# Kernel optimization log

Hardware: AMD Instinct MI355X
Metric: run time of the kernel (lower is better)

The kernel has to match this reference:

```python
import jax, jax.numpy as jnp
import numpy as np

NUM_HEADS = 8

def setup_inputs() -> dict:
    key = jax.random.key(0)
    k1, k2, k3, k4 = jax.random.split(key, 4)
    B, N, C = 2, 4096, 768
    x = jax.random.normal(k1, (B, N, C), dtype=jnp.float32)
    w_qkv = jax.random.normal(k2, (C, 3 * C), dtype=jnp.float32) * (C ** -0.5)
    w_proj = jax.random.normal(k3, (C, C), dtype=jnp.float32) * (C ** -0.5)
    b_proj = jax.random.normal(k4, (C,), dtype=jnp.float32) * 0.02
    return {"x": x, "w_qkv": w_qkv, "w_proj": w_proj, "b_proj": b_proj}

def reference(x, w_qkv, w_proj, b_proj):
    B, N, C = x.shape
    H = NUM_HEADS
    Dh = C // H
    scale = Dh ** -0.5
    # qkv: [B, N, 3C] -> [B, N, 3, H, Dh] -> [3, B, H, N, Dh]
    qkv = (x @ w_qkv).reshape(B, N, 3, H, Dh).transpose(2, 0, 3, 1, 4)
    q, k, v = qkv[0], qkv[1], qkv[2]
    attn = jnp.einsum('bhqd,bhkd->bhqk', q, k) * scale  # [B,H,N,N]
    attn = jax.nn.softmax(attn, axis=-1)
    out = jnp.einsum('bhqk,bhkd->bhqd', attn, v)        # [B,H,N,Dh]
    out = out.transpose(0, 2, 1, 3).reshape(B, N, C)
    return out @ w_proj + b_proj
```

## Files before the change

### kernel.cpp

```cpp
#include <hip/hip_runtime.h>
#include <hip/hip_bf16.h>

typedef __attribute__((ext_vector_type(8))) short short8;
typedef __attribute__((ext_vector_type(4))) short short4v;
typedef __attribute__((ext_vector_type(4))) float f32x4;
typedef __attribute__((ext_vector_type(16))) float f32x16;

#define MFMA16(a,b,c) __builtin_amdgcn_mfma_f32_16x16x32_bf16(a,b,c,0,0,0)
#define MFMA32(a,b,c) __builtin_amdgcn_mfma_f32_32x32x16_bf16(a,b,c,0,0,0)

__device__ __forceinline__ unsigned short f2b_rne(float f){
  union { float f; unsigned int u; } v; v.f = f;
  unsigned int u = v.u;
  return (unsigned short)((u + 0x7FFFu + ((u >> 16) & 1u)) >> 16);
}

__device__ __forceinline__ short8 pack8f(float4 a, float4 b){
  short8 o;
  o[0] = (short)f2b_rne(a.x); o[1] = (short)f2b_rne(a.y);
  o[2] = (short)f2b_rne(a.z); o[3] = (short)f2b_rne(a.w);
  o[4] = (short)f2b_rne(b.x); o[5] = (short)f2b_rne(b.y);
  o[6] = (short)f2b_rne(b.z); o[7] = (short)f2b_rne(b.w);
  return o;
}

__device__ __forceinline__ f32x16 zero16(){
  f32x16 z;
  #pragma unroll
  for (int i = 0; i < 16; ++i) z[i] = 0.f;
  return z;
}

__global__ void k_transpose_cvt2(const float* __restrict__ wqkv, const float* __restrict__ wproj,
                                 unsigned short* __restrict__ oqkv, unsigned short* __restrict__ oproj){
  __shared__ unsigned short tile[32][33];
  const float* in; unsigned short* out; int Cc;
  if (blockIdx.z == 0){ in = wqkv; out = oqkv; Cc = 2304; }
  else {
    if (blockIdx.x >= 24) return;
    in = wproj; out = oproj; Cc = 768;
  }
  int c0 = blockIdx.x * 32, r0 = blockIdx.y * 32;
  int tx = threadIdx.x, ty = threadIdx.y;
  #pragma unroll
  for (int i = 0; i < 32; i += 8)
    tile[ty + i][tx] = f2b_rne(in[(size_t)(r0 + ty + i) * Cc + c0 + tx]);
  __syncthreads();
  #pragma unroll
  for (int i = 0; i < 32; i += 8)
    out[(size_t)(c0 + ty + i) * 768 + r0 + tx] = tile[tx][ty + i];
}

__global__ __launch_bounds__(256) void k_gemm_qkv(
    const float* __restrict__ X,
    const unsigned short* __restrict__ Bt,
    unsigned short* __restrict__ qbuf,
    unsigned short* __restrict__ kbuf,
    unsigned short* __restrict__ vtb)
{
  __shared__ short As[128 * 40];
  __shared__ short Bs[128 * 40];
  int m0 = blockIdx.x * 128, n0 = blockIdx.y * 128;
  int t = threadIdx.x, l = t & 63, w = t >> 6;
  int lr = l & 15, lh = l >> 4;
  int wr = w >> 1, wc = w & 1;

  int row0 = t >> 2, cs0 = t & 3;
  int row1 = row0 + 64;
  const float* ga0 = X + (size_t)(m0 + row0) * 768 + cs0 * 8;
  const float* ga1 = X + (size_t)(m0 + row1) * 768 + cs0 * 8;
  const unsigned short* gb0 = Bt + (size_t)(n0 + row0) * 768 + cs0 * 8;
  const unsigned short* gb1 = Bt + (size_t)(n0 + row1) * 768 + cs0 * 8;
  short* la0 = As + row0 * 40 + cs0 * 8;
  short* la1 = As + row1 * 40 + cs0 * 8;
  short* lb0 = Bs + row0 * 40 + cs0 * 8;
  short* lb1 = Bs + row1 * 40 + cs0 * 8;

  f32x4 acc[4][4];
  f32x4 z4 = {0.f, 0.f, 0.f, 0.f};
  #pragma unroll
  for (int mf = 0; mf < 4; ++mf)
    #pragma unroll
    for (int nf = 0; nf < 4; ++nf) acc[mf][nf] = z4;

  float4 fa0 = *(const float4*)ga0, fa0b = *(const float4*)(ga0 + 4);
  float4 fa1 = *(const float4*)ga1, fa1b = *(const float4*)(ga1 + 4);
  short8 rb0 = *(const short8*)gb0;
  short8 rb1 = *(const short8*)gb1;

  for (int kt = 0; kt < 24; ++kt){
    short8 ra0 = pack8f(fa0, fa0b);
    short8 ra1 = pack8f(fa1, fa1b);
    __syncthreads();
    *(short8*)la0 = ra0; *(short8*)la1 = ra1;
    *(short8*)lb0 = rb0; *(short8*)lb1 = rb1;
    __syncthreads();
    if (kt < 23){
      fa0 = *(const float4*)(ga0 + (kt + 1) * 32); fa0b = *(const float4*)(ga0 + (kt + 1) * 32 + 4);
      fa1 = *(const float4*)(ga1 + (kt + 1) * 32); fa1b = *(const float4*)(ga1 + (kt + 1) * 32 + 4);
      rb0 = *(const short8*)(gb0 + (kt + 1) * 32);
      rb1 = *(const short8*)(gb1 + (kt + 1) * 32);
    }
    short8 af[4], bfm[4];
    #pragma unroll
    for (int mf = 0; mf < 4; ++mf)
      af[mf] = *(const short8*)(As + (wr * 64 + mf * 16 + lr) * 40 + lh * 8);
    #pragma unroll
    for (int nf = 0; nf < 4; ++nf)
      bfm[nf] = *(const short8*)(Bs + (wc * 64 + nf * 16 + lr) * 40 + lh * 8);
    #pragma unroll
    for (int mf = 0; mf < 4; ++mf)
      #pragma unroll
      for (int nf = 0; nf < 4; ++nf)
        acc[mf][nf] = MFMA16(af[mf], bfm[nf], acc[mf][nf]);
  }

  const float qscale = 0.10206207261596577f * 1.4426950408889634f;
  int three = n0 / 768;
  int b_ = m0 >> 12;
  int ntok0 = m0 & 4095;
  #pragma unroll
  for (int nf = 0; nf < 4; ++nf){
    int gcol = n0 + wc * 64 + nf * 16 + lr;
    int jj = gcol - three * 768;
    int h = jj / 96;
    int dh = jj - h * 96;
    #pragma unroll
    for (int mf = 0; mf < 4; ++mf){
      int ntok = ntok0 + wr * 64 + mf * 16 + lh * 4;
      if (three == 0){
        unsigned short* dst = qbuf + (size_t)(b_ * 8 + h) * 4096 * 96;
        #pragma unroll
        for (int r = 0; r < 4; ++r)
          dst[(size_t)(ntok + r) * 96 + dh] = f2b_rne(acc[mf][nf][r] * qscale);
      } else if (three == 1){
        unsigned short* dst = kbuf + (size_t)(b_ * 8 + h) * 4096 * 96;
        #pragma unroll
        for (int r = 0; r < 4; ++r)
          dst[(size_t)(ntok + r) * 96 + dh] = f2b_rne(acc[mf][nf][r]);
      } else {
        short4v sv;
        #pragma unroll
        for (int r = 0; r < 4; ++r) sv[r] = (short)f2b_rne(acc[mf][nf][r]);
        *(short4v*)(vtb + ((size_t)(b_ * 8 + h) * 96 + dh) * 4096 + ntok) = sv;
      }
    }
  }
}

__global__ __launch_bounds__(512) void k_attn12(
    const unsigned short* __restrict__ qb,
    const unsigned short* __restrict__ kb,
    const unsigned short* __restrict__ vtb,
    unsigned short* __restrict__ ao)
{
  __shared__ short lds[27136];
  const int bh = blockIdx.x;
  const int qt = blockIdx.y;
  const int tid = threadIdx.x;
  const int ln = tid & 63, wid = tid >> 6;
  const int qc = ln & 31, hi = ln >> 5;
  const int q0 = qt * 256 + wid * 32;

  const unsigned short* qbase = qb  + (size_t)bh * 4096 * 96;
  const unsigned short* kbase = kb  + (size_t)bh * 4096 * 96;
  const unsigned short* vbase = vtb + (size_t)bh * 96 * 4096;

  short8 qf[6];
  #pragma unroll
  for (int kw = 0; kw < 6; ++kw)
    qf[kw] = *(const short8*)(qbase + (size_t)(q0 + qc) * 96 + kw * 16 + hi * 8);

  const unsigned short* gp[3]; int gstep[3], loff[3], lstep[3];
  #pragma unroll
  for (int j = 0; j < 3; ++j){
    int c = tid + j * 512;
    if (c < 768){
      int r = c / 12, cl = c - r * 12;
      gp[j] = kbase + r * 96 + cl * 8; gstep[j] = 64 * 96;
      loff[j] = r * 104 + cl * 8;      lstep[j] = 6656;
    } else {
      int cv = c - 768; int r = cv >> 3, cl = cv & 7;
      gp[j] = vbase + (size_t)r * 4096 + cl * 8; gstep[j] = 64;
      loff[j] = 13312 + r * 72 + cl * 8;         lstep[j] = 6912;
    }
  }

  short8 rs[3];
  #pragma unroll
  for (int j = 0; j < 3; ++j){ rs[j] = *(const short8*)gp[j]; gp[j] += gstep[j]; }
  #pragma unroll
  for (int j = 0; j < 3; ++j) *(short8*)(lds + loff[j]) = rs[j];

  f32x16 oacc[3];
  #pragma unroll
  for (int dt = 0; dt < 3; ++dt) oacc[dt] = zero16();
  float lsum = 0.f;

  const int krd = qc * 104 + hi * 8;
  const int vrd = 13312 + qc * 72 + hi * 8;

#define CVTPK(d, lo_, hi_) asm("v_cvt_pk_bf16_f32 %0, %1, %2" : "=v"(d) : "v"(lo_), "v"(hi_))
#define PLSWAP(x_, y_)     asm("v_permlane32_swap_b32 %0, %1" : "+v"(x_), "+v"(y_))

  for (int kt = 0; kt < 64; ++kt){
    const int cur = kt & 1;
    __syncthreads();
    if (kt < 63){
      #pragma unroll
      for (int j = 0; j < 3; ++j){ rs[j] = *(const short8*)gp[j]; gp[j] += gstep[j]; }
    }
    const short* Kb = lds + cur * 6656 + krd;
    const short* Vb = lds + cur * 6912 + vrd;

    f32x16 s0 = zero16(), s1 = zero16();
    __builtin_amdgcn_s_setprio(1);
    #pragma unroll
    for (int kw = 0; kw < 6; ++kw){
      short8 kf = *(const short8*)(Kb + kw * 16);
      s0 = MFMA32(kf, qf[kw], s0);
    }
    #pragma unroll
    for (int kw = 0; kw < 6; ++kw){
      short8 kf = *(const short8*)(Kb + 3328 + kw * 16);
      s1 = MFMA32(kf, qf[kw], s1);
    }
    __builtin_amdgcn_s_setprio(0);

    {
      float p0 = 0.f, p1 = 0.f, p2 = 0.f, p3 = 0.f;
      #pragma unroll
      for (int r = 0; r < 16; r += 4){
        s0[r]   = exp2f(s0[r]   - 12.0f); p0 += s0[r];
        s0[r+1] = exp2f(s0[r+1] - 12.0f); p1 += s0[r+1];
        s0[r+2] = exp2f(s0[r+2] - 12.0f); p2 += s0[r+2];
        s0[r+3] = exp2f(s0[r+3] - 12.0f); p3 += s0[r+3];
      }
      #pragma unroll
      for (int r = 0; r < 16; r += 4){
        s1[r]   = exp2f(s1[r]   - 12.0f); p0 += s1[r];
        s1[r+1] = exp2f(s1[r+1] - 12.0f); p1 += s1[r+1];
        s1[r+2] = exp2f(s1[r+2] - 12.0f); p2 += s1[r+2];
        s1[r+3] = exp2f(s1[r+3] - 12.0f); p3 += s1[r+3];
      }
      lsum += (p0 + p1) + (p2 + p3);
    }

    short8 pa[4];
    {
      unsigned int a, b;
      union { unsigned int u[4]; short8 s; } pk;
      CVTPK(a, s0[0], s0[1]);  CVTPK(b, s0[4],  s0[5]);  PLSWAP(a, b); pk.u[0] = a; pk.u[2] = b;
      CVTPK(a, s0[2], s0[3]);  CVTPK(b, s0[6],  s0[7]);  PLSWAP(a, b); pk.u[1] = a; pk.u[3] = b;
      pa[0] = pk.s;
      CVTPK(a, s0[8], s0[9]);  CVTPK(b, s0[12], s0[13]); PLSWAP(a, b); pk.u[0] = a; pk.u[2] = b;
      CVTPK(a, s0[10], s0[11]); CVTPK(b, s0[14], s0[15]); PLSWAP(a, b); pk.u[1] = a; pk.u[3] = b;
      pa[1] = pk.s;
      CVTPK(a, s1[0], s1[1]);  CVTPK(b, s1[4],  s1[5]);  PLSWAP(a, b); pk.u[0] = a; pk.u[2] = b;
      CVTPK(a, s1[2], s1[3]);  CVTPK(b, s1[6],  s1[7]);  PLSWAP(a, b); pk.u[1] = a; pk.u[3] = b;
      pa[2] = pk.s;
      CVTPK(a, s1[8], s1[9]);  CVTPK(b, s1[12], s1[13]); PLSWAP(a, b); pk.u[0] = a; pk.u[2] = b;
      CVTPK(a, s1[10], s1[11]); CVTPK(b, s1[14], s1[15]); PLSWAP(a, b); pk.u[1] = a; pk.u[3] = b;
      pa[3] = pk.s;
    }

    __builtin_amdgcn_s_setprio(1);
    #pragma unroll
    for (int dt = 0; dt < 3; ++dt){
      #pragma unroll
      for (int w = 0; w < 4; ++w){
        short8 vf = *(const short8*)(Vb + dt * 2304 + w * 16);
        oacc[dt] = MFMA32(vf, pa[w], oacc[dt]);
      }
    }
    __builtin_amdgcn_s_setprio(0);

    if (kt < 63){
      const int nb = cur ^ 1;
      #pragma unroll
      for (int j = 0; j < 3; ++j) *(short8*)(lds + loff[j] + nb * lstep[j]) = rs[j];
    }
  }

  float lt = lsum + __shfl_xor(lsum, 32, 64);
  float inv = 1.0f / lt;
  int b_ = bh >> 3, h = bh & 7;
  unsigned short* orow = ao + (size_t)(b_ * 4096 + q0 + qc) * 768 + h * 96;
  #pragma unroll
  for (int dt = 0; dt < 3; ++dt)
    #pragma unroll
    for (int g = 0; g < 4; ++g){
      short4v sv;
      #pragma unroll
      for (int r = 0; r < 4; ++r) sv[r] = (short)f2b_rne(oacc[dt][g * 4 + r] * inv);
      *(short4v*)(orow + dt * 32 + g * 8 + hi * 4) = sv;
    }
#undef CVTPK
#undef PLSWAP
}

__global__ __launch_bounds__(256) void k_gemm_proj(
    const unsigned short* __restrict__ A,
    const unsigned short* __restrict__ Bt,
    const float* __restrict__ bias,
    float* __restrict__ out)
{
  __shared__ short As[128 * 40];
  __shared__ short Bs[128 * 40];
  int m0 = blockIdx.x * 128, n0 = blockIdx.y * 128;
  int t = threadIdx.x, l = t & 63, w = t >> 6;
  int lr = l & 15, lh = l >> 4;
  int wr = w >> 1, wc = w & 1;

  int row0 = t >> 2, cs0 = t & 3;
  int row1 = row0 + 64;
  const unsigned short* ga0 = A  + (size_t)(m0 + row0) * 768 + cs0 * 8;
  const unsigned short* ga1 = A  + (size_t)(m0 + row1) * 768 + cs0 * 8;
  const unsigned short* gb0 = Bt + (size_t)(n0 + row0) * 768 + cs0 * 8;
  const unsigned short* gb1 = Bt + (size_t)(n0 + row1) * 768 + cs0 * 8;
  short* la0 = As + row0 * 40 + cs0 * 8;
  short* la1 = As + row1 * 40 + cs0 * 8;
  short* lb0 = Bs + row0 * 40 + cs0 * 8;
  short* lb1 = Bs + row1 * 40 + cs0 * 8;

  f32x4 acc[4][4];
  f32x4 z4 = {0.f, 0.f, 0.f, 0.f};
  #pragma unroll
  for (int mf = 0; mf < 4; ++mf)
    #pragma unroll
    for (int nf = 0; nf < 4; ++nf) acc[mf][nf] = z4;

  short8 ra0 = *(const short8*)ga0;
  short8 ra1 = *(const short8*)ga1;
  short8 rb0 = *(const short8*)gb0;
  short8 rb1 = *(const short8*)gb1;

  for (int kt = 0; kt < 24; ++kt){
    __syncthreads();
    *(short8*)la0 = ra0; *(short8*)la1 = ra1;
    *(short8*)lb0 = rb0; *(short8*)lb1 = rb1;
    __syncthreads();
    if (kt < 23){
      ra0 = *(const short8*)(ga0 + (kt + 1) * 32);
      ra1 = *(const short8*)(ga1 + (kt + 1) * 32);
      rb0 = *(const short8*)(gb0 + (kt + 1) * 32);
      rb1 = *(const short8*)(gb1 + (kt + 1) * 32);
    }
    short8 af[4], bfm[4];
    #pragma unroll
    for (int mf = 0; mf < 4; ++mf)
      af[mf] = *(const short8*)(As + (wr * 64 + mf * 16 + lr) * 40 + lh * 8);
    #pragma unroll
    for (int nf = 0; nf < 4; ++nf)
      bfm[nf] = *(const short8*)(Bs + (wc * 64 + nf * 16 + lr) * 40 + lh * 8);
    #pragma unroll
    for (int mf = 0; mf < 4; ++mf)
      #pragma unroll
      for (int nf = 0; nf < 4; ++nf)
        acc[mf][nf] = MFMA16(af[mf], bfm[nf], acc[mf][nf]);
  }

  #pragma unroll
  for (int nf = 0; nf < 4; ++nf){
    int gcol = n0 + wc * 64 + nf * 16 + lr;
    float bb = bias[gcol];
    #pragma unroll
    for (int mf = 0; mf < 4; ++mf){
      int grow = m0 + wr * 64 + mf * 16 + lh * 4;
      #pragma unroll
      for (int r = 0; r < 4; ++r)
        out[(size_t)(grow + r) * 768 + gcol] = acc[mf][nf][r] + bb;
    }
  }
}

extern "C" void kernel_launch(void* const* d_in, const int* in_sizes, int n_in,
                              void* d_out, int out_size, void* d_ws, size_t ws_size,
                              hipStream_t stream) {
  const float* x      = (const float*)d_in[0];
  const float* w_qkv  = (const float*)d_in[1];
  const float* w_proj = (const float*)d_in[2];
  const float* b_proj = (const float*)d_in[3];
  float* out = (float*)d_out;
  char* ws = (char*)d_ws;

  unsigned short* aob    = (unsigned short*)(ws);
  unsigned short* wqkvt  = (unsigned short*)(ws + 12582912);
  unsigned short* wprojt = (unsigned short*)(ws + 16121856);
  unsigned short* qbuf   = (unsigned short*)(ws + 17301504);
  unsigned short* kbuf   = (unsigned short*)(ws + 29884416);
  unsigned short* vtb    = (unsigned short*)(ws + 42467328);

  k_transpose_cvt2<<<dim3(72, 24, 2), dim3(32, 8), 0, stream>>>(w_qkv, w_proj, wqkvt, wprojt);
  k_gemm_qkv<<<dim3(64, 18), 256, 0, stream>>>(x, wqkvt, qbuf, kbuf, vtb);
  k_attn12<<<dim3(16, 16), 512, 0, stream>>>(qbuf, kbuf, vtb, aob);
  k_gemm_proj<<<dim3(64, 6), 256, 0, stream>>>(aob, wprojt, b_proj, out);
}
```

Before: 216.2 us.

## Software-pipeline attention: overlap PV MFMAs of previous tile with QK of current

Restructures the attention inner loop so the P·V MFMAs for key tile kt-1 are issued in the same high-priority block as the Q·K MFMAs for tile kt. The exp/softmax VALU work then has independent matrix work beside it. V is triple-buffered in LDS (rotating prev/cur/next offsets) while K stays double-buffered, and a final epilogue performs the last PV product. This costs more LDS and keeps the packed P fragments live across iterations, which raises register pressure.

```diff
diff --git a/kernel.cpp b/kernel.cpp
--- a/kernel.cpp
+++ b/kernel.cpp
@@ -148,13 +148,13 @@
   }
 }
 
-__global__ __launch_bounds__(512) void k_attn12(
+__global__ __launch_bounds__(512) void k_attn15(
     const unsigned short* __restrict__ qb,
     const unsigned short* __restrict__ kb,
     const unsigned short* __restrict__ vtb,
     unsigned short* __restrict__ ao)
 {
-  __shared__ short lds[27136];
+  __shared__ short lds[34048];
   const int bh = blockIdx.x;
   const int qt = blockIdx.y;
   const int tid = threadIdx.x;
@@ -171,18 +171,18 @@
   for (int kw = 0; kw < 6; ++kw)
     qf[kw] = *(const short8*)(qbase + (size_t)(q0 + qc) * 96 + kw * 16 + hi * 8);
 
-  const unsigned short* gp[3]; int gstep[3], loff[3], lstep[3];
+  const unsigned short* gp[3]; int gstep[3], loff[3], isV[3];
   #pragma unroll
   for (int j = 0; j < 3; ++j){
     int c = tid + j * 512;
     if (c < 768){
       int r = c / 12, cl = c - r * 12;
       gp[j] = kbase + r * 96 + cl * 8; gstep[j] = 64 * 96;
-      loff[j] = r * 104 + cl * 8;      lstep[j] = 6656;
+      loff[j] = r * 104 + cl * 8;      isV[j] = 0;
     } else {
       int cv = c - 768; int r = cv >> 3, cl = cv & 7;
       gp[j] = vbase + (size_t)r * 4096 + cl * 8; gstep[j] = 64;
-      loff[j] = 13312 + r * 72 + cl * 8;         lstep[j] = 6912;
+      loff[j] = r * 72 + cl * 8;                 isV[j] = 1;
     }
   }
 
@@ -190,7 +190,7 @@
   #pragma unroll
   for (int j = 0; j < 3; ++j){ rs[j] = *(const short8*)gp[j]; gp[j] += gstep[j]; }
   #pragma unroll
-  for (int j = 0; j < 3; ++j) *(short8*)(lds + loff[j]) = rs[j];
+  for (int j = 0; j < 3; ++j) *(short8*)(lds + loff[j] + (isV[j] ? 13312 : 0)) = rs[j];
 
   f32x16 oacc[3];
   #pragma unroll
@@ -198,20 +198,22 @@
   float lsum = 0.f;
 
   const int krd = qc * 104 + hi * 8;
-  const int vrd = 13312 + qc * 72 + hi * 8;
+  const int vrd = qc * 72 + hi * 8;
+
+  int vprev = 13312 + 2 * 6912, vcur = 13312, vnext = 13312 + 6912;
+
+  short8 pa[4];
 
 #define CVTPK(d, lo_, hi_) asm("v_cvt_pk_bf16_f32 %0, %1, %2" : "=v"(d) : "v"(lo_), "v"(hi_))
 #define PLSWAP(x_, y_)     asm("v_permlane32_swap_b32 %0, %1" : "+v"(x_), "+v"(y_))
 
   for (int kt = 0; kt < 64; ++kt){
-    const int cur = kt & 1;
     __syncthreads();
     if (kt < 63){
       #pragma unroll
       for (int j = 0; j < 3; ++j){ rs[j] = *(const short8*)gp[j]; gp[j] += gstep[j]; }
     }
-    const short* Kb = lds + cur * 6656 + krd;
-    const short* Vb = lds + cur * 6912 + vrd;
+    const short* Kb = lds + (kt & 1) * 6656 + krd;
 
     f32x16 s0 = zero16(), s1 = zero16();
     __builtin_amdgcn_s_setprio(1);
@@ -224,6 +226,17 @@
     for (int kw = 0; kw < 6; ++kw){
       short8 kf = *(const short8*)(Kb + 3328 + kw * 16);
       s1 = MFMA32(kf, qf[kw], s1);
+    }
+    if (kt > 0){
+      const short* Vb = lds + vprev + vrd;
+      #pragma unroll
+      for (int dt = 0; dt < 3; ++dt){
+        #pragma unroll
+        for (int w = 0; w < 4; ++w){
+          short8 vf = *(const short8*)(Vb + dt * 2304 + w * 16);
+          oacc[dt] = MFMA32(vf, pa[w], oacc[dt]);
+        }
+      }
     }
     __builtin_amdgcn_s_setprio(0);
 
@@ -246,7 +259,6 @@
       lsum += (p0 + p1) + (p2 + p3);
     }
 
-    short8 pa[4];
     {
       unsigned int a, b;
       union { unsigned int u[4]; short8 s; } pk;
@@ -264,6 +276,18 @@
       pa[3] = pk.s;
     }
 
+    if (kt < 63){
+      const int kwb = ((kt + 1) & 1) * 6656;
+      #pragma unroll
+      for (int j = 0; j < 3; ++j)
+        *(short8*)(lds + loff[j] + (isV[j] ? vnext : kwb)) = rs[j];
+    }
+
+    int tmpv = vprev; vprev = vcur; vcur = vnext; vnext = tmpv;
+  }
+
+  {
+    const short* Vb = lds + vprev + vrd;
     __builtin_amdgcn_s_setprio(1);
     #pragma unroll
     for (int dt = 0; dt < 3; ++dt){
@@ -274,12 +298,6 @@
       }
     }
     __builtin_amdgcn_s_setprio(0);
-
-    if (kt < 63){
-      const int nb = cur ^ 1;
-      #pragma unroll
-      for (int j = 0; j < 3; ++j) *(short8*)(lds + loff[j] + nb * lstep[j]) = rs[j];
-    }
   }
 
   float lt = lsum + __shfl_xor(lsum, 32, 64);
@@ -393,6 +411,6 @@
 
   k_transpose_cvt2<<<dim3(72, 24, 2), dim3(32, 8), 0, stream>>>(w_qkv, w_proj, wqkvt, wprojt);
   k_gemm_qkv<<<dim3(64, 18), 256, 0, stream>>>(x, wqkvt, qbuf, kbuf, vtb);
-  k_attn12<<<dim3(16, 16), 512, 0, stream>>>(qbuf, kbuf, vtb, aob);
+  k_attn15<<<dim3(16, 16), 512, 0, stream>>>(qbuf, kbuf, vtb, aob);
   k_gemm_proj<<<dim3(64, 6), 256, 0, stream>>>(aob, wprojt, b_proj, out);
 }
```

New measurement: 217.0 us. No clear change (+0.4%).
